# Optimization experiments

Measured on AMD Instinct MI355X. Metric: run time of the kernel, lower is better.

## Reference

```python
import jax, jax.numpy as jnp
import numpy as np

L, E, TOP_K = 3, 8, 2
B, N, D, DS = 256, 1024, 512, 128

def setup_inputs() -> dict:
    key = jax.random.key(0)
    ks = jax.random.split(key, 10)
    s = 0.05  # weight init scale
    return {
        "token": jax.random.normal(ks[0], (B, 1, D), jnp.float32),
        "node_emb": jax.random.normal(ks[1], (B, N, D), jnp.float32),
        "states": jnp.zeros((L, E, B, DS), jnp.float32),
        "Wg": jax.random.normal(ks[2], (L, D, E), jnp.float32) * s,
        "bg": jnp.zeros((L, E), jnp.float32),
        "A": jax.random.normal(ks[3], (L, E, DS), jnp.float32),
        "Bin": jax.random.normal(ks[4], (L, E, D, DS), jnp.float32) * s,
        "Cout": jax.random.normal(ks[5], (L, E, DS, D), jnp.float32) * s,
        "Dsk": jax.random.normal(ks[6], (L, E, D), jnp.float32) * s,
        "Wq": jax.random.normal(ks[7], (D, D), jnp.float32) * s,
        "bq": jnp.zeros((D,), jnp.float32),
    }

def reference(token, node_emb, states, Wg, bg, A, Bin, Cout, Dsk, Wq, bq):
    # token: (B,1,D) -> h: (B,D)
    h = token[:, 0, :]
    lb_loss = jnp.float32(0.0)
    new_states = []
    for l in range(L):
        # --- MoE router: top-k softmax gating ---
        probs = jax.nn.softmax(h @ Wg[l] + bg[l])              # (B,E)
        topv, topi = jax.lax.top_k(probs, TOP_K)               # (B,k)
        gates_k = topv / jnp.sum(topv, axis=-1, keepdims=True)  # renormalized
        oh = jax.nn.one_hot(topi, E, dtype=probs.dtype)        # (B,k,E)
        gate_full = jnp.einsum('bk,bke->be', gates_k, oh)      # (B,E)
        sel = jnp.sum(oh, axis=1) > 0                          # (B,E) bool
        # --- state-space experts (computed densely for all experts) ---
        s = states[l]                                          # (E,B,DS)
        decay = jax.nn.sigmoid(A[l])[:, None, :]               # (E,1,DS)
        s_new = decay * s + jnp.einsum('bd,eds->ebs', h, Bin[l])   # (E,B,DS)
        y = jnp.einsum('ebs,esd->ebd', s_new, Cout[l]) + h[None] * Dsk[l][:, None, :]
        out = jnp.einsum('be,ebd->bd', gate_full, y)           # weighted combine
        # only routed experts advance their state
        keep = sel.T[:, :, None]                               # (E,B,1)
        new_states.append(jnp.where(keep, s_new, s))
        # load-balance loss: E * sum_e mean(probs_e) * mean(frac routed to e)
        lb_loss = lb_loss + E * jnp.sum(jnp.mean(probs, axis=0) * jnp.mean(sel.astype(probs.dtype), axis=0))
        h = h + out                                            # residual
    # --- query projection + logits over nodes ---
    q = h @ Wq + bq                                            # (B,D)
    logits = jnp.einsum('bd,bnd->bn', q, node_emb) / jnp.sqrt(jnp.float32(D))
    return logits, jnp.stack(new_states), lb_loss
```

## Files before the change

kernel.cpp:

```cpp
#include <hip/hip_runtime.h>
#include <math.h>

#define LNUM 3
#define ENUM 8
#define BSZ 256
#define NSZ 1024
#define DSZ 512
#define SSZ 128

typedef float f32x4 __attribute__((ext_vector_type(4)));

__global__ __launch_bounds__(512, 4) void layer2_kernel(
    const float* __restrict__ h_base,
    const float* __restrict__ y_in,
    float* __restrict__ h_store,
    float* __restrict__ y_out,
    const float* __restrict__ Wg_l,
    const float* __restrict__ bg_l,
    const float* __restrict__ A_l,
    const float* __restrict__ Bin_l,
    const float* __restrict__ Cou_l,
    const float* __restrict__ Dsk_l,
    const float* __restrict__ st_l,
    float* __restrict__ os_l,
    float* __restrict__ acc_probs,
    float* __restrict__ acc_sel)
{
    const int b = blockIdx.x & 255;
    const int k = blockIdx.x >> 8;
    const int t = threadIdx.x;
    const int wave = t >> 6;
    const int lane = t & 63;

    __shared__ float h_s[DSZ];
    __shared__ float snew_s[SSZ];
    __shared__ float logit_s[ENUM];
    __shared__ f32x4 part4[512];
    float* part = (float*)part4;

    if (t < 128) {
        f32x4 hq = ((const f32x4*)(h_base + (size_t)b * DSZ))[t];
        if (y_in) {
            hq += ((const f32x4*)(y_in + (size_t)b * DSZ))[t];
            hq += ((const f32x4*)(y_in + (size_t)(BSZ + b) * DSZ))[t];
        }
        ((f32x4*)h_s)[t] = hq;
        if (h_store && k == 0) ((f32x4*)(h_store + (size_t)b * DSZ))[t] = hq;
    }
    __syncthreads();

    {
        float p = 0.f;
        #pragma unroll
        for (int i = 0; i < 8; ++i) {
            const int d = lane + i * 64;
            p = fmaf(h_s[d], Wg_l[d * ENUM + wave], p);
        }
        for (int off = 32; off; off >>= 1) p += __shfl_down(p, off, 64);
        if (lane == 0) logit_s[wave] = p + bg_l[wave];
    }
    __syncthreads();

    float probs[ENUM];
    float mx = logit_s[0];
    for (int e = 1; e < ENUM; ++e) mx = fmaxf(mx, logit_s[e]);
    float ssum = 0.f;
    for (int e = 0; e < ENUM; ++e) { probs[e] = expf(logit_s[e] - mx); ssum += probs[e]; }
    const float sinv = 1.f / ssum;
    for (int e = 0; e < ENUM; ++e) probs[e] *= sinv;

    int i0 = 0;
    for (int e = 1; e < ENUM; ++e) if (probs[e] > probs[i0]) i0 = e;
    int i1 = -1;
    for (int e = 0; e < ENUM; ++e) {
        if (e == i0) continue;
        if (i1 < 0 || probs[e] > probs[i1]) i1 = e;
    }
    float g0 = probs[i0], g1 = probs[i1];
    const float ginv = 1.f / (g0 + g1);
    g0 *= ginv; g1 *= ginv;

    if (k == 0 && t < ENUM) {
        atomicAdd(&acc_probs[t], probs[t]);
        atomicAdd(&acc_sel[t], (t == i0 || t == i1) ? 1.0f : 0.0f);
    }

    const int esel = k ? i1 : i0;
    const float gsel = k ? g1 : g0;

    {
        const int kc = t >> 5, sq = t & 31;
        const float* Bp = Bin_l + (size_t)esel * DSZ * SSZ + sq * 4;
        const int d0 = kc * 32;
        f32x4 a4 = {0.f, 0.f, 0.f, 0.f};
        #pragma unroll
        for (int d = 0; d < 32; ++d)
            a4 += *(const f32x4*)(Bp + (size_t)(d0 + d) * SSZ) * h_s[d0 + d];
        part4[t] = a4;
    }
    __syncthreads();

    if (t < SSZ) {
        float sum = 0.f;
        #pragma unroll
        for (int kc = 0; kc < 16; ++kc) sum += part[kc * 128 + t];
        const float a = A_l[esel * SSZ + t];
        const float decay = 1.f / (1.f + expf(-a));
        snew_s[t] = decay * st_l[((size_t)esel * BSZ + b) * SSZ + t] + sum;
    }
    __syncthreads();

    if (t < SSZ) os_l[((size_t)esel * BSZ + b) * SSZ + t] = snew_s[t];
    {
        const int e = k * 4 + (t >> 7);
        const int s = t & 127;
        if (e != i0 && e != i1)
            os_l[((size_t)e * BSZ + b) * SSZ + s] = st_l[((size_t)e * BSZ + b) * SSZ + s];
    }

    {
        const int sc = t >> 7, dq = t & 127;
        const float* Cp = Cou_l + (size_t)esel * SSZ * DSZ + dq * 4;
        const int s0 = sc * 32;
        f32x4 a4 = {0.f, 0.f, 0.f, 0.f};
        #pragma unroll
        for (int s = 0; s < 32; ++s)
            a4 += *(const f32x4*)(Cp + (size_t)(s0 + s) * DSZ) * snew_s[s0 + s];
        part4[sc * 128 + dq] = a4;
    }
    __syncthreads();

    if (t < 128) {
        f32x4 yq = part4[t] + part4[128 + t] + part4[256 + t] + part4[384 + t];
        const f32x4 hq = ((const f32x4*)h_s)[t];
        const f32x4 dk = *(const f32x4*)(Dsk_l + esel * DSZ + t * 4);
        yq += hq * dk;
        ((f32x4*)(y_out + (size_t)(k * BSZ + b) * DSZ))[t] = yq * gsel;
    }
}

__global__ __launch_bounds__(512, 4) void q2_kernel(
    const float* __restrict__ h_base,
    const float* __restrict__ y_in,
    const float* __restrict__ Wq,
    const float* __restrict__ bq,
    float* __restrict__ q_out)
{
    const int b = blockIdx.x & 255;
    const int k = blockIdx.x >> 8;
    const int t = threadIdx.x;

    __shared__ float h_s[DSZ];
    __shared__ f32x4 part4[512];

    if (t < 128) {
        f32x4 hq = ((const f32x4*)(h_base + (size_t)b * DSZ))[t]
                 + ((const f32x4*)(y_in + (size_t)b * DSZ))[t]
                 + ((const f32x4*)(y_in + (size_t)(BSZ + b) * DSZ))[t];
        ((f32x4*)h_s)[t] = hq;
    }
    __syncthreads();

    {
        const int kc = t >> 6, cq = t & 63;
        const float* Wp = Wq + k * 256 + cq * 4;
        const int d0 = kc * 64;
        f32x4 a4 = {0.f, 0.f, 0.f, 0.f};
        #pragma unroll
        for (int i = 0; i < 64; ++i)
            a4 += *(const f32x4*)(Wp + (size_t)(d0 + i) * DSZ) * h_s[d0 + i];
        part4[kc * 64 + cq] = a4;
    }
    __syncthreads();

    if (t < 64) {
        f32x4 qq = *(const f32x4*)(bq + k * 256 + t * 4);
        #pragma unroll
        for (int kc = 0; kc < 8; ++kc) qq += part4[kc * 64 + t];
        ((f32x4*)(q_out + (size_t)b * DSZ))[k * 64 + t] = qq;
    }
}

__global__ __launch_bounds__(256) void logits_kernel(
    const float* __restrict__ q, const float* __restrict__ node_emb,
    float* __restrict__ logits,
    const float* __restrict__ acc, float* __restrict__ loss_out)
{
    const int b = blockIdx.y;
    const int wave = threadIdx.x >> 6;
    const int lane = threadIdx.x & 63;

    if (blockIdx.x == 0 && blockIdx.y == 0 && threadIdx.x == 0) {
        float lb = 0.f;
        for (int l = 0; l < LNUM; ++l)
            for (int e = 0; e < ENUM; ++e) {
                const float mp = acc[(l * 2 + 0) * ENUM + e] * (1.0f / BSZ);
                const float ms = acc[(l * 2 + 1) * ENUM + e] * (1.0f / BSZ);
                lb += (float)ENUM * mp * ms;
            }
        loss_out[0] = lb;
    }

    const f32x4* q4 = (const f32x4*)(q + b * DSZ);
    const f32x4 q0 = q4[lane];
    const f32x4 q1 = q4[lane + 64];
    const float scale = 0.04419417382415922f;

    const int n0 = blockIdx.x * 128 + wave * 32;
    #pragma unroll 2
    for (int i = 0; i < 32; ++i) {
        const int n = n0 + i;
        const f32x4* r = (const f32x4*)(node_emb + ((size_t)b * NSZ + n) * DSZ);
        const f32x4 a0 = __builtin_nontemporal_load(&r[lane]);
        const f32x4 a1 = __builtin_nontemporal_load(&r[lane + 64]);
        float dot = a0.x * q0.x + a0.y * q0.y + a0.z * q0.z + a0.w * q0.w
                  + a1.x * q1.x + a1.y * q1.y + a1.z * q1.z + a1.w * q1.w;
        for (int off = 32; off; off >>= 1) dot += __shfl_down(dot, off, 64);
        if (lane == 0) logits[b * NSZ + n] = dot * scale;
    }
}

extern "C" void kernel_launch(void* const* d_in, const int* in_sizes, int n_in,
                              void* d_out, int out_size, void* d_ws, size_t ws_size,
                              hipStream_t stream) {
    const float* token    = (const float*)d_in[0];
    const float* node_emb = (const float*)d_in[1];
    const float* states   = (const float*)d_in[2];
    const float* Wg       = (const float*)d_in[3];
    const float* bg       = (const float*)d_in[4];
    const float* A        = (const float*)d_in[5];
    const float* Bin      = (const float*)d_in[6];
    const float* Cout     = (const float*)d_in[7];
    const float* Dsk      = (const float*)d_in[8];
    const float* Wq       = (const float*)d_in[9];
    const float* bq       = (const float*)d_in[10];

    float* out_logits = (float*)d_out;
    float* out_states = out_logits + (size_t)BSZ * NSZ;
    float* out_loss   = out_states + (size_t)LNUM * ENUM * BSZ * SSZ;

    float* ws_q   = (float*)d_ws;
    float* ws_acc = ws_q + (size_t)BSZ * DSZ;
    float* hbuf0  = ws_acc + 64;
    float* hbuf1  = hbuf0 + (size_t)BSZ * DSZ;
    float* ybufA  = hbuf1 + (size_t)BSZ * DSZ;
    float* ybufB  = ybufA + (size_t)2 * BSZ * DSZ;

    (void)hipMemsetAsync(ws_acc, 0, sizeof(float) * LNUM * 16, stream);

    const float* y_ins[LNUM]   = { nullptr, ybufA, ybufB };
    float*       h_stores[LNUM]= { nullptr, hbuf0, hbuf1 };
    float*       y_outs[LNUM]  = { ybufA,   ybufB, ybufA };
    const float* h_bases[LNUM] = { token,   token, hbuf0 };

    for (int l = 0; l < LNUM; ++l) {
        layer2_kernel<<<512, 512, 0, stream>>>(
            h_bases[l], y_ins[l], h_stores[l], y_outs[l],
            Wg  + (size_t)l * DSZ * ENUM,
            bg  + (size_t)l * ENUM,
            A   + (size_t)l * ENUM * SSZ,
            Bin + (size_t)l * ENUM * DSZ * SSZ,
            Cout+ (size_t)l * ENUM * SSZ * DSZ,
            Dsk + (size_t)l * ENUM * DSZ,
            states + (size_t)l * ENUM * BSZ * SSZ,
            out_states + (size_t)l * ENUM * BSZ * SSZ,
            ws_acc + (l * 2 + 0) * ENUM,
            ws_acc + (l * 2 + 1) * ENUM);
    }

    q2_kernel<<<512, 512, 0, stream>>>(hbuf1, ybufA, Wq, bq, ws_q);

    dim3 lg(NSZ / 128, BSZ);
    logits_kernel<<<lg, 256, 0, stream>>>(ws_q, node_emb, out_logits, ws_acc, out_loss);
}
```

Before: 184.2 us.

## Group tokens by routed expert to reuse expert weights across token tiles

Replaces the per-token, per-slot layer kernel with three kernels per layer. A gate kernel computes routing for 8 tokens per block and builds per-expert token lists. A state kernel and an output kernel then process up to 32 tokens of the same expert per block, so Bin and Cout rows are loaded once and reused across those tokens instead of being re-read by every token block. The skip term h*Dsk is folded into the next layer's h reconstruction, the query projection is batched over 8 tokens, and the logits loop processes two node rows per iteration. The cost is more kernel launches, atomics-based list building whose token order is nondeterministic, and idle blocks when expert loads are uneven.

```diff
diff --git a/kernel.cpp b/kernel.cpp
--- a/kernel.cpp
+++ b/kernel.cpp
@@ -7,178 +7,277 @@
 #define NSZ 1024
 #define DSZ 512
 #define SSZ 128
+#define HPAD 516
 
 typedef float f32x4 __attribute__((ext_vector_type(4)));
 
-__global__ __launch_bounds__(512, 4) void layer2_kernel(
+__global__ __launch_bounds__(256) void gate_kernel(
     const float* __restrict__ h_base,
     const float* __restrict__ y_in,
-    float* __restrict__ h_store,
-    float* __restrict__ y_out,
+    const float* __restrict__ gates_prev,
+    const float* __restrict__ Dsk_prev,
+    float* __restrict__ hbuf,
     const float* __restrict__ Wg_l,
     const float* __restrict__ bg_l,
+    const float* __restrict__ st_l,
+    float* __restrict__ os_l,
+    float* __restrict__ gates_l,
+    int* __restrict__ cnt_l,
+    int* __restrict__ list_l,
+    float* __restrict__ acc_probs,
+    float* __restrict__ acc_sel)
+{
+    const int t = threadIdx.x;
+    const int b0 = blockIdx.x * 8;
+
+    __shared__ float h_s[8 * HPAD];
+    __shared__ float wg_s[DSZ * ENUM];
+    __shared__ float dsk_s[ENUM * DSZ];
+    __shared__ float gprev_s[8 * ENUM];
+    __shared__ float lgp[256];
+    __shared__ float lg_s[8][ENUM];
+    __shared__ int   sel_s[8][2];
+    __shared__ float psum[ENUM], ssum[ENUM];
+
+    for (int i = t; i < 1024; i += 256) ((f32x4*)wg_s)[i] = ((const f32x4*)Wg_l)[i];
+    if (y_in) {
+        for (int i = t; i < 1024; i += 256) ((f32x4*)dsk_s)[i] = ((const f32x4*)Dsk_prev)[i];
+        if (t < 64) gprev_s[t] = gates_prev[b0 * ENUM + t];
+    }
+    if (t < ENUM) { psum[t] = 0.f; ssum[t] = 0.f; }
+    __syncthreads();
+
+    for (int i = t; i < 1024; i += 256) {
+        const int tok = i >> 7, dq = i & 127;
+        const int b = b0 + tok;
+        f32x4 hq = ((const f32x4*)(h_base + (size_t)b * DSZ))[dq];
+        if (y_in) {
+            f32x4 w = {0.f, 0.f, 0.f, 0.f};
+            #pragma unroll
+            for (int e = 0; e < ENUM; ++e)
+                w += ((const f32x4*)(dsk_s + e * DSZ))[dq] * gprev_s[tok * ENUM + e];
+            hq = hq + hq * w
+               + ((const f32x4*)(y_in + (size_t)b * DSZ))[dq]
+               + ((const f32x4*)(y_in + (size_t)(BSZ + b) * DSZ))[dq];
+        }
+        *(f32x4*)(h_s + tok * HPAD + dq * 4) = hq;
+        ((f32x4*)(hbuf + (size_t)b * DSZ))[dq] = hq;
+    }
+    __syncthreads();
+
+    {
+        const int tok = t >> 5, e = (t >> 2) & 7, qt = t & 3;
+        const float* hp = h_s + tok * HPAD + qt * 128;
+        const float* wp = wg_s + (qt * 128) * ENUM + e;
+        float p = 0.f;
+        #pragma unroll 8
+        for (int d = 0; d < 128; ++d) p = fmaf(hp[d], wp[d * ENUM], p);
+        lgp[t] = p;
+    }
+    __syncthreads();
+    if (t < 64) {
+        const int tok = t >> 3, e = t & 7;
+        lg_s[tok][e] = lgp[tok * 32 + e * 4] + lgp[tok * 32 + e * 4 + 1]
+                     + lgp[tok * 32 + e * 4 + 2] + lgp[tok * 32 + e * 4 + 3] + bg_l[e];
+    }
+    __syncthreads();
+
+    if (t < 8) {
+        const int b = b0 + t;
+        float probs[ENUM];
+        float mx = lg_s[t][0];
+        for (int e = 1; e < ENUM; ++e) mx = fmaxf(mx, lg_s[t][e]);
+        float ss = 0.f;
+        for (int e = 0; e < ENUM; ++e) { probs[e] = expf(lg_s[t][e] - mx); ss += probs[e]; }
+        const float sinv = 1.f / ss;
+        for (int e = 0; e < ENUM; ++e) probs[e] *= sinv;
+        int i0 = 0;
+        for (int e = 1; e < ENUM; ++e) if (probs[e] > probs[i0]) i0 = e;
+        int i1 = -1;
+        for (int e = 0; e < ENUM; ++e) {
+            if (e == i0) continue;
+            if (i1 < 0 || probs[e] > probs[i1]) i1 = e;
+        }
+        const float gs = 1.f / (probs[i0] + probs[i1]);
+        for (int e = 0; e < ENUM; ++e) {
+            float g = 0.f;
+            if (e == i0) g = probs[i0] * gs;
+            else if (e == i1) g = probs[i1] * gs;
+            gates_l[b * ENUM + e] = g;
+            atomicAdd(&psum[e], probs[e]);
+        }
+        atomicAdd(&ssum[i0], 1.0f);
+        atomicAdd(&ssum[i1], 1.0f);
+        sel_s[t][0] = i0; sel_s[t][1] = i1;
+        const int idx0 = atomicAdd(&cnt_l[i0], 1);
+        list_l[i0 * 256 + idx0] = b;
+        const int idx1 = atomicAdd(&cnt_l[i1], 1);
+        list_l[i1 * 256 + idx1] = b | (1 << 8);
+    }
+    __syncthreads();
+    if (t < ENUM) {
+        atomicAdd(&acc_probs[t], psum[t]);
+        atomicAdd(&acc_sel[t], ssum[t]);
+    }
+
+    for (int i = t; i < 2048; i += 256) {
+        const int e = i >> 8, tok = (i >> 5) & 7, sq = i & 31;
+        if (e == sel_s[tok][0] || e == sel_s[tok][1]) continue;
+        const size_t off = ((size_t)e * BSZ + (b0 + tok)) * SSZ;
+        ((f32x4*)(os_l + off))[sq] = ((const f32x4*)(st_l + off))[sq];
+    }
+}
+
+__global__ __launch_bounds__(1024, 1) void snew_kernel(
+    const float* __restrict__ hbuf,
     const float* __restrict__ A_l,
     const float* __restrict__ Bin_l,
-    const float* __restrict__ Cou_l,
-    const float* __restrict__ Dsk_l,
     const float* __restrict__ st_l,
     float* __restrict__ os_l,
-    float* __restrict__ acc_probs,
-    float* __restrict__ acc_sel)
-{
-    const int b = blockIdx.x & 255;
-    const int k = blockIdx.x >> 8;
+    const int* __restrict__ cnt_l,
+    const int* __restrict__ list_l)
+{
+    const int e = blockIdx.x & 7, tile = (blockIdx.x >> 3) & 7, sc = blockIdx.x >> 6;
+    const int ntot = cnt_l[e];
+    const int base = tile * 32;
+    if (base >= ntot) return;
+    const int nt = min(32, ntot - base);
     const int t = threadIdx.x;
-    const int wave = t >> 6;
-    const int lane = t & 63;
-
-    __shared__ float h_s[DSZ];
-    __shared__ float snew_s[SSZ];
-    __shared__ float logit_s[ENUM];
-    __shared__ f32x4 part4[512];
-    float* part = (float*)part4;
-
-    if (t < 128) {
-        f32x4 hq = ((const f32x4*)(h_base + (size_t)b * DSZ))[t];
-        if (y_in) {
-            hq += ((const f32x4*)(y_in + (size_t)b * DSZ))[t];
-            hq += ((const f32x4*)(y_in + (size_t)(BSZ + b) * DSZ))[t];
-        }
-        ((f32x4*)h_s)[t] = hq;
-        if (h_store && k == 0) ((f32x4*)(h_store + (size_t)b * DSZ))[t] = hq;
-    }
-    __syncthreads();
-
+
+    __shared__ float h_s[32][DSZ];
+    __shared__ int toks[32];
+
+    if (t < 32) toks[t] = (t < nt) ? (list_l[e * 256 + base + t] & 255) : 0;
+    __syncthreads();
+    for (int i = t; i < 32 * 128; i += 1024) {
+        const int tok = i >> 7, dq = i & 127;
+        ((f32x4*)h_s[tok])[dq] = ((const f32x4*)(hbuf + (size_t)toks[tok] * DSZ))[dq];
+    }
+    __syncthreads();
+
+    const int tok = t >> 5, s = t & 31;
+    if (tok < nt) {
+        const int sglob = sc * 32 + s;
+        const float* hp = h_s[tok];
+        const float* Bp = Bin_l + (size_t)e * DSZ * SSZ + sglob;
+        float a0 = 0.f, a1 = 0.f, a2 = 0.f, a3 = 0.f;
+        #pragma unroll 8
+        for (int d = 0; d < 512; d += 4) {
+            a0 = fmaf(hp[d + 0], Bp[(size_t)(d + 0) * SSZ], a0);
+            a1 = fmaf(hp[d + 1], Bp[(size_t)(d + 1) * SSZ], a1);
+            a2 = fmaf(hp[d + 2], Bp[(size_t)(d + 2) * SSZ], a2);
+            a3 = fmaf(hp[d + 3], Bp[(size_t)(d + 3) * SSZ], a3);
+        }
+        const float sum = (a0 + a1) + (a2 + a3);
+        const int b = toks[tok];
+        const float a = A_l[e * SSZ + sglob];
+        const float decay = 1.f / (1.f + expf(-a));
+        const float sn = decay * st_l[((size_t)e * BSZ + b) * SSZ + sglob] + sum;
+        os_l[((size_t)e * BSZ + b) * SSZ + sglob] = sn;
+    }
+}
+
+__global__ __launch_bounds__(1024, 1) void y_kernel(
+    const float* __restrict__ os_l,
+    const float* __restrict__ Cou_l,
+    const float* __restrict__ gates_l,
+    float* __restrict__ ybuf,
+    const int* __restrict__ cnt_l,
+    const int* __restrict__ list_l)
+{
+    const int e = blockIdx.x & 7, tile = (blockIdx.x >> 3) & 7, dc = blockIdx.x >> 6;
+    const int ntot = cnt_l[e];
+    const int base = tile * 32;
+    if (base >= ntot) return;
+    const int nt = min(32, ntot - base);
+    const int t = threadIdx.x;
+
+    __shared__ float sn_s[32][SSZ];
+    __shared__ int toks[32], slots[32];
+    __shared__ float g_s[32];
+
+    if (t < 32) {
+        const int entry = (t < nt) ? list_l[e * 256 + base + t] : 0;
+        toks[t] = entry & 255;
+        slots[t] = (entry >> 8) & 1;
+        g_s[t] = gates_l[(entry & 255) * ENUM + e];
+    }
+    __syncthreads();
     {
-        float p = 0.f;
-        #pragma unroll
-        for (int i = 0; i < 8; ++i) {
-            const int d = lane + i * 64;
-            p = fmaf(h_s[d], Wg_l[d * ENUM + wave], p);
-        }
-        for (int off = 32; off; off >>= 1) p += __shfl_down(p, off, 64);
-        if (lane == 0) logit_s[wave] = p + bg_l[wave];
-    }
-    __syncthreads();
-
-    float probs[ENUM];
-    float mx = logit_s[0];
-    for (int e = 1; e < ENUM; ++e) mx = fmaxf(mx, logit_s[e]);
-    float ssum = 0.f;
-    for (int e = 0; e < ENUM; ++e) { probs[e] = expf(logit_s[e] - mx); ssum += probs[e]; }
-    const float sinv = 1.f / ssum;
-    for (int e = 0; e < ENUM; ++e) probs[e] *= sinv;
-
-    int i0 = 0;
-    for (int e = 1; e < ENUM; ++e) if (probs[e] > probs[i0]) i0 = e;
-    int i1 = -1;
-    for (int e = 0; e < ENUM; ++e) {
-        if (e == i0) continue;
-        if (i1 < 0 || probs[e] > probs[i1]) i1 = e;
-    }
-    float g0 = probs[i0], g1 = probs[i1];
-    const float ginv = 1.f / (g0 + g1);
-    g0 *= ginv; g1 *= ginv;
-
-    if (k == 0 && t < ENUM) {
-        atomicAdd(&acc_probs[t], probs[t]);
-        atomicAdd(&acc_sel[t], (t == i0 || t == i1) ? 1.0f : 0.0f);
-    }
-
-    const int esel = k ? i1 : i0;
-    const float gsel = k ? g1 : g0;
-
-    {
-        const int kc = t >> 5, sq = t & 31;
-        const float* Bp = Bin_l + (size_t)esel * DSZ * SSZ + sq * 4;
-        const int d0 = kc * 32;
-        f32x4 a4 = {0.f, 0.f, 0.f, 0.f};
-        #pragma unroll
-        for (int d = 0; d < 32; ++d)
-            a4 += *(const f32x4*)(Bp + (size_t)(d0 + d) * SSZ) * h_s[d0 + d];
-        part4[t] = a4;
-    }
-    __syncthreads();
-
-    if (t < SSZ) {
-        float sum = 0.f;
-        #pragma unroll
-        for (int kc = 0; kc < 16; ++kc) sum += part[kc * 128 + t];
-        const float a = A_l[esel * SSZ + t];
-        const float decay = 1.f / (1.f + expf(-a));
-        snew_s[t] = decay * st_l[((size_t)esel * BSZ + b) * SSZ + t] + sum;
-    }
-    __syncthreads();
-
-    if (t < SSZ) os_l[((size_t)esel * BSZ + b) * SSZ + t] = snew_s[t];
-    {
-        const int e = k * 4 + (t >> 7);
-        const int s = t & 127;
-        if (e != i0 && e != i1)
-            os_l[((size_t)e * BSZ + b) * SSZ + s] = st_l[((size_t)e * BSZ + b) * SSZ + s];
-    }
-
-    {
-        const int sc = t >> 7, dq = t & 127;
-        const float* Cp = Cou_l + (size_t)esel * SSZ * DSZ + dq * 4;
-        const int s0 = sc * 32;
-        f32x4 a4 = {0.f, 0.f, 0.f, 0.f};
-        #pragma unroll
-        for (int s = 0; s < 32; ++s)
-            a4 += *(const f32x4*)(Cp + (size_t)(s0 + s) * DSZ) * snew_s[s0 + s];
-        part4[sc * 128 + dq] = a4;
-    }
-    __syncthreads();
-
-    if (t < 128) {
-        f32x4 yq = part4[t] + part4[128 + t] + part4[256 + t] + part4[384 + t];
-        const f32x4 hq = ((const f32x4*)h_s)[t];
-        const f32x4 dk = *(const f32x4*)(Dsk_l + esel * DSZ + t * 4);
-        yq += hq * dk;
-        ((f32x4*)(y_out + (size_t)(k * BSZ + b) * DSZ))[t] = yq * gsel;
-    }
-}
-
-__global__ __launch_bounds__(512, 4) void q2_kernel(
-    const float* __restrict__ h_base,
-    const float* __restrict__ y_in,
+        const int tok = t >> 5, sq = t & 31;
+        ((f32x4*)sn_s[tok])[sq] =
+            ((const f32x4*)(os_l + ((size_t)e * BSZ + toks[tok]) * SSZ))[sq];
+    }
+    __syncthreads();
+
+    const int tok = t >> 5, dq = t & 31;
+    if (tok < nt) {
+        const int dcb = dc * 128;
+        const float* Cp = Cou_l + (size_t)e * SSZ * DSZ + dcb + dq * 4;
+        const float* snp = sn_s[tok];
+        f32x4 A0 = {0.f,0.f,0.f,0.f}, A1 = A0, A2 = A0, A3 = A0;
+        #pragma unroll 8
+        for (int s = 0; s < 128; s += 4) {
+            A0 += *(const f32x4*)(Cp + (size_t)(s + 0) * DSZ) * snp[s + 0];
+            A1 += *(const f32x4*)(Cp + (size_t)(s + 1) * DSZ) * snp[s + 1];
+            A2 += *(const f32x4*)(Cp + (size_t)(s + 2) * DSZ) * snp[s + 2];
+            A3 += *(const f32x4*)(Cp + (size_t)(s + 3) * DSZ) * snp[s + 3];
+        }
+        const f32x4 y4 = ((A0 + A1) + (A2 + A3)) * g_s[tok];
+        ((f32x4*)(ybuf + (size_t)(slots[tok] * BSZ + toks[tok]) * DSZ + dcb))[dq] = y4;
+    }
+}
+
+__global__ __launch_bounds__(256) void q_kernel(
+    const float* __restrict__ hbuf,
+    const float* __restrict__ ybuf,
+    const float* __restrict__ gates2,
+    const float* __restrict__ Dsk2,
     const float* __restrict__ Wq,
     const float* __restrict__ bq,
     float* __restrict__ q_out)
 {
-    const int b = blockIdx.x & 255;
-    const int k = blockIdx.x >> 8;
     const int t = threadIdx.x;
-
-    __shared__ float h_s[DSZ];
-    __shared__ f32x4 part4[512];
-
-    if (t < 128) {
-        f32x4 hq = ((const f32x4*)(h_base + (size_t)b * DSZ))[t]
-                 + ((const f32x4*)(y_in + (size_t)b * DSZ))[t]
-                 + ((const f32x4*)(y_in + (size_t)(BSZ + b) * DSZ))[t];
-        ((f32x4*)h_s)[t] = hq;
-    }
-    __syncthreads();
-
-    {
-        const int kc = t >> 6, cq = t & 63;
-        const float* Wp = Wq + k * 256 + cq * 4;
-        const int d0 = kc * 64;
-        f32x4 a4 = {0.f, 0.f, 0.f, 0.f};
+    const int b0 = (blockIdx.x & 31) * 8;
+    const int colb = (blockIdx.x >> 5) * 128;
+
+    __shared__ float h_s[8 * HPAD];
+    __shared__ float dsk_s[ENUM * DSZ];
+    __shared__ float gprev_s[8 * ENUM];
+
+    for (int i = t; i < 1024; i += 256) ((f32x4*)dsk_s)[i] = ((const f32x4*)Dsk2)[i];
+    if (t < 64) gprev_s[t] = gates2[b0 * ENUM + t];
+    __syncthreads();
+
+    for (int i = t; i < 1024; i += 256) {
+        const int tok = i >> 7, dq = i & 127;
+        const int b = b0 + tok;
+        f32x4 hq = ((const f32x4*)(hbuf + (size_t)b * DSZ))[dq];
+        f32x4 w = {0.f, 0.f, 0.f, 0.f};
         #pragma unroll
-        for (int i = 0; i < 64; ++i)
-            a4 += *(const f32x4*)(Wp + (size_t)(d0 + i) * DSZ) * h_s[d0 + i];
-        part4[kc * 64 + cq] = a4;
-    }
-    __syncthreads();
-
-    if (t < 64) {
-        f32x4 qq = *(const f32x4*)(bq + k * 256 + t * 4);
-        #pragma unroll
-        for (int kc = 0; kc < 8; ++kc) qq += part4[kc * 64 + t];
-        ((f32x4*)(q_out + (size_t)b * DSZ))[k * 64 + t] = qq;
-    }
+        for (int e = 0; e < ENUM; ++e)
+            w += ((const f32x4*)(dsk_s + e * DSZ))[dq] * gprev_s[tok * ENUM + e];
+        hq = hq + hq * w
+           + ((const f32x4*)(ybuf + (size_t)b * DSZ))[dq]
+           + ((const f32x4*)(ybuf + (size_t)(BSZ + b) * DSZ))[dq];
+        *(f32x4*)(h_s + tok * HPAD + dq * 4) = hq;
+    }
+    __syncthreads();
+
+    const int tok = t >> 5, cq = t & 31;
+    const float* hp = h_s + tok * HPAD;
+    const float* Wp = Wq + colb + cq * 4;
+    f32x4 A0 = {0.f,0.f,0.f,0.f}, A1 = A0, A2 = A0, A3 = A0;
+    #pragma unroll 8
+    for (int d = 0; d < 512; d += 4) {
+        A0 += *(const f32x4*)(Wp + (size_t)(d + 0) * DSZ) * hp[d + 0];
+        A1 += *(const f32x4*)(Wp + (size_t)(d + 1) * DSZ) * hp[d + 1];
+        A2 += *(const f32x4*)(Wp + (size_t)(d + 2) * DSZ) * hp[d + 2];
+        A3 += *(const f32x4*)(Wp + (size_t)(d + 3) * DSZ) * hp[d + 3];
+    }
+    f32x4 q4 = (A0 + A1) + (A2 + A3);
+    q4 += *(const f32x4*)(bq + colb + cq * 4);
+    ((f32x4*)(q_out + (size_t)(b0 + tok) * DSZ))[colb / 4 + cq] = q4;
 }
 
 __global__ __launch_bounds__(256) void logits_kernel(
@@ -194,8 +293,8 @@
         float lb = 0.f;
         for (int l = 0; l < LNUM; ++l)
             for (int e = 0; e < ENUM; ++e) {
-                const float mp = acc[(l * 2 + 0) * ENUM + e] * (1.0f / BSZ);
-                const float ms = acc[(l * 2 + 1) * ENUM + e] * (1.0f / BSZ);
+                const float mp = acc[l * 16 + e] * (1.0f / BSZ);
+                const float ms = acc[l * 16 + 8 + e] * (1.0f / BSZ);
                 lb += (float)ENUM * mp * ms;
             }
         loss_out[0] = lb;
@@ -207,16 +306,26 @@
     const float scale = 0.04419417382415922f;
 
     const int n0 = blockIdx.x * 128 + wave * 32;
-    #pragma unroll 2
-    for (int i = 0; i < 32; ++i) {
-        const int n = n0 + i;
-        const f32x4* r = (const f32x4*)(node_emb + ((size_t)b * NSZ + n) * DSZ);
-        const f32x4 a0 = __builtin_nontemporal_load(&r[lane]);
-        const f32x4 a1 = __builtin_nontemporal_load(&r[lane + 64]);
-        float dot = a0.x * q0.x + a0.y * q0.y + a0.z * q0.z + a0.w * q0.w
-                  + a1.x * q1.x + a1.y * q1.y + a1.z * q1.z + a1.w * q1.w;
-        for (int off = 32; off; off >>= 1) dot += __shfl_down(dot, off, 64);
-        if (lane == 0) logits[b * NSZ + n] = dot * scale;
+    for (int i = 0; i < 32; i += 2) {
+        const f32x4* r0 = (const f32x4*)(node_emb + ((size_t)b * NSZ + n0 + i) * DSZ);
+        const f32x4* r1 = (const f32x4*)(node_emb + ((size_t)b * NSZ + n0 + i + 1) * DSZ);
+        const f32x4 a0 = __builtin_nontemporal_load(r0 + lane);
+        const f32x4 a1 = __builtin_nontemporal_load(r0 + lane + 64);
+        const f32x4 c0 = __builtin_nontemporal_load(r1 + lane);
+        const f32x4 c1 = __builtin_nontemporal_load(r1 + lane + 64);
+        float d0 = a0.x*q0.x + a0.y*q0.y + a0.z*q0.z + a0.w*q0.w
+                 + a1.x*q1.x + a1.y*q1.y + a1.z*q1.z + a1.w*q1.w;
+        float d1 = c0.x*q0.x + c0.y*q0.y + c0.z*q0.z + c0.w*q0.w
+                 + c1.x*q1.x + c1.y*q1.y + c1.z*q1.z + c1.w*q1.w;
+        #pragma unroll
+        for (int off = 32; off; off >>= 1) {
+            d0 += __shfl_down(d0, off, 64);
+            d1 += __shfl_down(d1, off, 64);
+        }
+        if (lane == 0) {
+            logits[b * NSZ + n0 + i]     = d0 * scale;
+            logits[b * NSZ + n0 + i + 1] = d1 * scale;
+        }
     }
 }
 
@@ -239,37 +348,46 @@
     float* out_states = out_logits + (size_t)BSZ * NSZ;
     float* out_loss   = out_states + (size_t)LNUM * ENUM * BSZ * SSZ;
 
-    float* ws_q   = (float*)d_ws;
-    float* ws_acc = ws_q + (size_t)BSZ * DSZ;
-    float* hbuf0  = ws_acc + 64;
-    float* hbuf1  = hbuf0 + (size_t)BSZ * DSZ;
-    float* ybufA  = hbuf1 + (size_t)BSZ * DSZ;
-    float* ybufB  = ybufA + (size_t)2 * BSZ * DSZ;
-
-    (void)hipMemsetAsync(ws_acc, 0, sizeof(float) * LNUM * 16, stream);
-
-    const float* y_ins[LNUM]   = { nullptr, ybufA, ybufB };
-    float*       h_stores[LNUM]= { nullptr, hbuf0, hbuf1 };
-    float*       y_outs[LNUM]  = { ybufA,   ybufB, ybufA };
-    const float* h_bases[LNUM] = { token,   token, hbuf0 };
+    float* ws_q    = (float*)d_ws;
+    float* hbuf    = ws_q + 131072;
+    float* ybuf    = hbuf + 131072;
+    float* gates   = ybuf + 262144;
+    int*   cnt     = (int*)(gates + 6144);
+    float* acc     = (float*)(cnt + 32);
+    int*   lists   = (int*)(acc + 64);
+
+    (void)hipMemsetAsync(cnt, 0, 384, stream);
 
     for (int l = 0; l < LNUM; ++l) {
-        layer2_kernel<<<512, 512, 0, stream>>>(
-            h_bases[l], y_ins[l], h_stores[l], y_outs[l],
-            Wg  + (size_t)l * DSZ * ENUM,
-            bg  + (size_t)l * ENUM,
-            A   + (size_t)l * ENUM * SSZ,
-            Bin + (size_t)l * ENUM * DSZ * SSZ,
-            Cout+ (size_t)l * ENUM * SSZ * DSZ,
-            Dsk + (size_t)l * ENUM * DSZ,
-            states + (size_t)l * ENUM * BSZ * SSZ,
-            out_states + (size_t)l * ENUM * BSZ * SSZ,
-            ws_acc + (l * 2 + 0) * ENUM,
-            ws_acc + (l * 2 + 1) * ENUM);
-    }
-
-    q2_kernel<<<512, 512, 0, stream>>>(hbuf1, ybufA, Wq, bq, ws_q);
+        const float* Wg_l  = Wg + (size_t)l * DSZ * ENUM;
+        const float* bg_l  = bg + (size_t)l * ENUM;
+        const float* A_l   = A + (size_t)l * ENUM * SSZ;
+        const float* Bin_l = Bin + (size_t)l * ENUM * DSZ * SSZ;
+        const float* Cou_l = Cout + (size_t)l * ENUM * SSZ * DSZ;
+        const float* st_l  = states + (size_t)l * ENUM * BSZ * SSZ;
+        float* os_l        = out_states + (size_t)l * ENUM * BSZ * SSZ;
+        float* gates_l     = gates + l * 2048;
+        int*   cnt_l       = cnt + l * 8;
+        int*   list_l      = lists + l * 2048;
+
+        gate_kernel<<<32, 256, 0, stream>>>(
+            (l == 0) ? token : hbuf,
+            (l == 0) ? nullptr : ybuf,
+            (l == 0) ? nullptr : gates + (l - 1) * 2048,
+            (l == 0) ? nullptr : Dsk + (size_t)(l - 1) * ENUM * DSZ,
+            hbuf, Wg_l, bg_l, st_l, os_l, gates_l, cnt_l, list_l,
+            acc + l * 16, acc + l * 16 + 8);
+
+        snew_kernel<<<256, 1024, 0, stream>>>(
+            hbuf, A_l, Bin_l, st_l, os_l, cnt_l, list_l);
+
+        y_kernel<<<256, 1024, 0, stream>>>(
+            os_l, Cou_l, gates_l, ybuf, cnt_l, list_l);
+    }
+
+    q_kernel<<<128, 256, 0, stream>>>(
+        hbuf, ybuf, gates + 2 * 2048, Dsk + (size_t)2 * ENUM * DSZ, Wq, bq, ws_q);
 
     dim3 lg(NSZ / 128, BSZ);
-    logits_kernel<<<lg, 256, 0, stream>>>(ws_q, node_emb, out_logits, ws_acc, out_loss);
-}
+    logits_kernel<<<lg, 256, 0, stream>>>(ws_q, node_emb, out_logits, acc, out_loss);
+}
```

Result: slower. 280.8 us (+52.4%).
